# Optimization experiments

Hardware: AMD Instinct MI355X
Metric: run time of the kernel (lower is better)

Reference implementation:

```python
import jax, jax.numpy as jnp
import numpy as np

# Config constants (match init_kwargs)
H = 1024   # hidden_size
F = 4096   # intermediate_size
E = 8      # num_moe_experts
K = 2      # moe_router_topk
S, B = 1024, 2  # seq_len, micro-batch


def setup_inputs() -> dict:
    key = jax.random.key(0)
    ks = jax.random.split(key, 6)
    return {
        "hidden_states": jax.random.normal(ks[0], (S, B, H), jnp.float32),
        "router_w": jax.random.normal(ks[1], (H, E), jnp.float32) * 0.02,
        "w1": jax.random.normal(ks[2], (E, H, F), jnp.float32) * 0.02,
        "b1": jax.random.normal(ks[3], (E, F), jnp.float32) * 0.02,
        "w2": jax.random.normal(ks[4], (E, F, H), jnp.float32) * 0.02,
        "b2": jax.random.normal(ks[5], (E, H), jnp.float32) * 0.02,
    }


def reference(hidden_states, router_w, w1, b1, w2, b2):
    S_, B_, H_ = hidden_states.shape
    x = hidden_states.reshape(-1, H_)                      # [N, H]
    N = x.shape[0]

    # --- TopKRouter (aux_loss routing): topk over logits, softmax over top-k logits ---
    logits = x @ router_w                                  # [N, E]
    top_logits, indices = jax.lax.top_k(logits, K)         # [N, K]
    scores = jax.nn.softmax(top_logits.astype(jnp.float32), axis=-1).astype(logits.dtype)

    # Combine weights [N, E]: scatter top-k scores into expert slots.
    combine = jnp.zeros((N, E), x.dtype).at[jnp.arange(N)[:, None], indices].add(scores)

    # --- Experts: per-expert GPTNeoXMLP (dense over all tokens; math-equivalent
    # to dispatch (token_permutation) + grouped GEMM + scatter_add combine
    # (token_unpermutation) with score weighting for topk>1) ---
    h = jax.nn.gelu(jnp.einsum('nh,ehf->enf', x, w1) + b1[:, None, :], approximate=False)
    y = jnp.einsum('enf,efh->enh', h, w2) + b2[:, None, :]  # [E, N, H]

    out = jnp.einsum('ne,enh->nh', combine, y)              # weighted combine
    return out.reshape(S_, B_, H_)
```

## Files before the change

### kernel.cpp

```cpp
#include <hip/hip_runtime.h>
#include <cmath>


#define H_DIM 1024
#define F_DIM 4096
#define E_NUM 8
#define N_TOK 2048
#define BK 64
#define MAX_SLOTS 5120
#define MAX_MT (MAX_SLOTS / 128)
#define G1_GRID (MAX_MT * 32)
#define G2_GRID (MAX_MT * 16)
#define CVT_BLKS 2048
#define WCHUNKS (E_NUM * H_DIM * F_DIM / 8)
#define XCHUNKS (N_TOK * H_DIM / 8)

typedef short s16x4 __attribute__((ext_vector_type(4)));
typedef short s16x8 __attribute__((ext_vector_type(8)));
typedef float f32x4 __attribute__((ext_vector_type(4)));
typedef __attribute__((address_space(3))) const unsigned short* lds_us;

__device__ __forceinline__ unsigned short f2bf(float f) {
  unsigned int u = __float_as_uint(f);
  u += 0x7fffu + ((u >> 16) & 1u);
  return (unsigned short)(u >> 16);
}

__device__ __forceinline__ void gload_lds16(const void* g, void* l) {
  __builtin_amdgcn_global_load_lds(
      (const __attribute__((address_space(1))) unsigned int*)g,
      (__attribute__((address_space(3))) unsigned int*)l, 16, 0, 0);
}

__device__ __forceinline__ int xcd_swz(int orig, int nwg) {
  const int cpx = nwg >> 3;
  return (orig & 7) * cpx + (orig >> 3);
}

__device__ __forceinline__ float fast_gelu(float v) {
  const float w = v * (1.0f + 0.044715f * v * v);
  const float t = __expf(-1.5957691216f * w);
  return v / (1.0f + t);
}

template<int OFS>
__device__ __forceinline__ s16x4 trread(lds_us p) {
  s16x4 r;
  asm volatile("ds_read_b64_tr_b16 %0, %1 offset:%2" : "=v"(r) : "v"(p), "i"(OFS));
  return r;
}

template<int KB>
__device__ __forceinline__ void ld_b4(lds_us bp, s16x8 bb[4]) {
  s16x4 p0 = trread<KB + 0>(bp),    q0 = trread<KB + 512>(bp);
  s16x4 p1 = trread<KB + 1024>(bp), q1 = trread<KB + 1536>(bp);
  s16x4 p2 = trread<KB + 2048>(bp), q2 = trread<KB + 2560>(bp);
  s16x4 p3 = trread<KB + 3072>(bp), q3 = trread<KB + 3584>(bp);
  bb[0] = __builtin_shufflevector(p0, q0, 0, 1, 2, 3, 4, 5, 6, 7);
  bb[1] = __builtin_shufflevector(p1, q1, 0, 1, 2, 3, 4, 5, 6, 7);
  bb[2] = __builtin_shufflevector(p2, q2, 0, 1, 2, 3, 4, 5, 6, 7);
  bb[3] = __builtin_shufflevector(p3, q3, 0, 1, 2, 3, 4, 5, 6, 7);
}

template<int KB>
__device__ __forceinline__ void ld_b2(lds_us bp, s16x8 bb[2]) {
  s16x4 p0 = trread<KB + 0>(bp),    q0 = trread<KB + 512>(bp);
  s16x4 p1 = trread<KB + 1024>(bp), q1 = trread<KB + 1536>(bp);
  bb[0] = __builtin_shufflevector(p0, q0, 0, 1, 2, 3, 4, 5, 6, 7);
  bb[1] = __builtin_shufflevector(p1, q1, 0, 1, 2, 3, 4, 5, 6, 7);
}

__device__ __forceinline__ void cvt_stream(const float* __restrict__ in,
                                           unsigned short* __restrict__ out,
                                           int blk, int nblk, int nchunks) {
  const int step = nblk * 256;
#pragma unroll 2
  for (int c = blk * 256 + threadIdx.x; c < nchunks; c += step) {
    const size_t i = (size_t)c * 8;
    f32x4 a = *(const f32x4*)(in + i);
    f32x4 b = *(const f32x4*)(in + i + 4);
    s16x8 u;
#pragma unroll
    for (int j = 0; j < 4; ++j) { u[j] = (short)f2bf(a[j]); u[4 + j] = (short)f2bf(b[j]); }
    *(s16x8*)&out[i] = u;
  }
}

__global__ __launch_bounds__(256) void prep_k(
    const float* __restrict__ w1, unsigned short* __restrict__ wbf1,
    const float* __restrict__ x, unsigned short* __restrict__ xb,
    const float* __restrict__ rw, int* __restrict__ topk_e, float* __restrict__ topk_s) {
  const int b = blockIdx.x;
  const int t = threadIdx.x;
  if (b < CVT_BLKS) { cvt_stream(w1, wbf1, b, CVT_BLKS, WCHUNKS); return; }
  if (b < CVT_BLKS + 128) { cvt_stream(x, xb, b - CVT_BLKS, 128, XCHUNKS); return; }
  const int n = (b - CVT_BLKS - 128) * 4 + (t >> 6);
  const int l = t & 63;
  float part[E_NUM];
#pragma unroll
  for (int e = 0; e < E_NUM; ++e) part[e] = 0.f;
  const float* xr = x + (size_t)n * H_DIM;
  for (int h = l; h < H_DIM; h += 64) {
    const float xv = xr[h];
    const float* rwr = rw + h * E_NUM;
#pragma unroll
    for (int e = 0; e < E_NUM; ++e) part[e] += xv * rwr[e];
  }
#pragma unroll
  for (int e = 0; e < E_NUM; ++e) {
#pragma unroll
    for (int off = 32; off > 0; off >>= 1) part[e] += __shfl_down(part[e], off);
  }
  if (l == 0) {
    float v0 = -3.4e38f, v1 = -3.4e38f;
    int i0 = 0, i1 = 0;
#pragma unroll
    for (int e = 0; e < E_NUM; ++e) {
      float v = part[e];
      if (v > v0) { v1 = v0; i1 = i0; v0 = v; i0 = e; }
      else if (v > v1) { v1 = v; i1 = e; }
    }
    const float e1 = expf(v1 - v0);
    const float inv = 1.f / (1.f + e1);
    topk_e[2 * n] = i0; topk_e[2 * n + 1] = i1;
    topk_s[2 * n] = inv; topk_s[2 * n + 1] = e1 * inv;
  }
}

__global__ __launch_bounds__(256) void scatter_k(
    int* __restrict__ meta, const int* __restrict__ topk_e,
    const float* __restrict__ topk_s, int* __restrict__ slot_token,
    float* __restrict__ slot_score) {
  __shared__ int cnt[4][8];
  __shared__ int soff[9];
  __shared__ int scur[8];
  const int t = threadIdx.x;
  const int wv = t >> 6;
  if (t < 32) cnt[t >> 3][t & 7] = 0;
  if (t < 8) scur[t] = 0;
  __syncthreads();
  for (int a = t; a < N_TOK * 2; a += 256)
    atomicAdd(&cnt[wv][topk_e[a]], 1);
  __syncthreads();
  if (t == 0) {
    int acc = 0;
    for (int e = 0; e < E_NUM; ++e) {
      const int c = cnt[0][e] + cnt[1][e] + cnt[2][e] + cnt[3][e];
      soff[e] = acc;
      meta[8 + e] = acc;
      acc += ((c + 127) / 128) * 128;
    }
    soff[8] = acc;
    meta[16] = acc;
  }
  __syncthreads();
  for (int a = t; a < N_TOK * 2; a += 256) {
    const int e = topk_e[a];
    const int pos = atomicAdd(&scur[e], 1);
    const int slot = soff[e] + pos;
    slot_token[slot] = a >> 1;
    slot_score[slot] = topk_s[a];
  }
}

#define KLANE(l) (((l) >> 3 & 3) * 8 + ((l) >> 5) * 4 + (((l) & 7) >> 1))

__global__ __launch_bounds__(256, 2) void gemm1_f(
    const unsigned short* __restrict__ xb, const unsigned short* __restrict__ wbf1,
    const float* __restrict__ b1, const int* __restrict__ meta,
    const int* __restrict__ slot_token, unsigned short* __restrict__ hbuf,
    const float* __restrict__ w2, unsigned short* __restrict__ wbf2) {
  __shared__ __align__(16) unsigned short Al[2 * 8192];
  __shared__ __align__(16) unsigned short Bl[2 * 8192];
  if (blockIdx.x >= G1_GRID) {
    cvt_stream(w2, wbf2, blockIdx.x - G1_GRID, CVT_BLKS, WCHUNKS);
    return;
  }
  const int total = meta[16];
  const int wgid = xcd_swz(blockIdx.x, G1_GRID);
  const int mt = wgid >> 5, nt = wgid & 31;
  const int m0 = mt * 128;
  if (m0 >= total) return;
  int exp = 0;
#pragma unroll
  for (int e = 1; e < E_NUM; ++e) if (m0 >= meta[8 + e]) exp = e;
  const int n0 = nt * 128;
  const int t = threadIdx.x, w = t >> 6, l = t & 63;
  const int wm = w >> 1, wn = w & 1, lr = l & 15, lg = l >> 4;
  const int sr = l >> 3, sc = l & 7;

  const unsigned short* srcA[4];
#pragma unroll
  for (int i = 0; i < 4; ++i) {
    const int r = (w * 4 + i) * 8 + sr;
    int tk = slot_token[m0 + r]; if (tk < 0) tk = 0;
    srcA[i] = xb + (size_t)tk * H_DIM + (sc ^ sr) * 8;
  }
  const unsigned short* wbe = wbf1 + (size_t)exp * H_DIM * F_DIM;
  const unsigned short* srcB[4];
#pragma unroll
  for (int i = 0; i < 4; ++i) {
    const int ri = w * 4 + i;
    const int kl = (ri >> 3) * 32 + KLANE(l);
    srcB[i] = wbe + (size_t)kl * F_DIM + n0 + (ri & 7) * 16 + (l & 1) * 8;
  }

  const f32x4 fzero = {0.f, 0.f, 0.f, 0.f};
  f32x4 acc[4][4];
#pragma unroll
  for (int a = 0; a < 4; ++a)
#pragma unroll
    for (int b = 0; b < 4; ++b) acc[a][b] = fzero;

#define GLA1(kt, Ad)                                                        \
  _Pragma("unroll") for (int i = 0; i < 4; ++i)                             \
      gload_lds16(srcA[i] + (kt) * BK, (Ad) + (w * 4 + i) * 512);
#define GLB1(kt, Bd)                                                        \
  _Pragma("unroll") for (int i = 0; i < 4; ++i)                             \
      gload_lds16(srcB[i] + (size_t)(kt) * (BK * F_DIM), (Bd) + (w * 4 + i) * 512);
#define MFMA1(Ac, Bc)                                                       \
  {                                                                         \
    lds_us bp = (lds_us)(Bc) + wn * 2048 + l * 4;                           \
    _Pragma("unroll") for (int kk = 0; kk < 2; ++kk) {                      \
      s16x8 af[4], bb[4];                                                   \
      _Pragma("unroll") for (int fm = 0; fm < 4; ++fm) {                    \
        const int row = wm * 64 + fm * 16 + lr;                             \
        af[fm] = *(const s16x8*)&(Ac)[row * 64 + (((kk * 4 + lg) ^ (lr & 7)) * 8)]; \
      }                                                                     \
      if (kk == 0) ld_b4<0>(bp, bb); else ld_b4<8192>(bp, bb);              \
      asm volatile("s_waitcnt lgkmcnt(0)" ::: "memory");                    \
      __builtin_amdgcn_sched_barrier(0);                                    \
      _Pragma("unroll") for (int fm = 0; fm < 4; ++fm)                      \
        _Pragma("unroll") for (int fn = 0; fn < 4; ++fn)                    \
          acc[fm][fn] = __builtin_amdgcn_mfma_f32_16x16x32_bf16(af[fm], bb[fn], acc[fm][fn], 0, 0, 0); \
    }                                                                       \
  }

  const int NT = H_DIM / BK;
  GLA1(0, Al) GLB1(0, Bl)
  __syncthreads();
  int cur = 0;
  for (int kt = 0; kt < NT; ++kt) {
    const int nxt = cur ^ 1;
    if (kt + 1 < NT) { GLA1(kt + 1, Al + nxt * 8192) GLB1(kt + 1, Bl + nxt * 8192) }
    MFMA1(Al + cur * 8192, Bl + cur * 8192)
    __syncthreads();
    cur = nxt;
  }
#pragma unroll
  for (int fn = 0; fn < 4; ++fn) {
    const int col = n0 + wn * 64 + fn * 16 + lr;
    const float bias = b1[exp * F_DIM + col];
#pragma unroll
    for (int fm = 0; fm < 4; ++fm) {
      const int rbase = m0 + wm * 64 + fm * 16 + lg * 4;
#pragma unroll
      for (int i = 0; i < 4; ++i) {
        hbuf[(size_t)(rbase + i) * F_DIM + col] = f2bf(fast_gelu(acc[fm][fn][i] + bias));
      }
    }
  }
}

__global__ __launch_bounds__(256, 3) void gemm2_f(
    const unsigned short* __restrict__ hbuf, const unsigned short* __restrict__ wbf2,
    const float* __restrict__ b2, const int* __restrict__ meta,
    const int* __restrict__ slot_token, const float* __restrict__ slot_score,
    float* __restrict__ out) {
  __shared__ __align__(16) unsigned short Al[2 * 8192];
  __shared__ __align__(16) unsigned short Bl[2 * 4096];
  const int total = meta[16];
  const int wgid = xcd_swz(blockIdx.x, G2_GRID);
  const int mt = wgid >> 4, nt = wgid & 15;
  const int m0 = mt * 128;
  if (m0 >= total) return;
  int exp = 0;
#pragma unroll
  for (int e = 1; e < E_NUM; ++e) if (m0 >= meta[8 + e]) exp = e;
  const int n0 = nt * 64;
  const int t = threadIdx.x, w = t >> 6, l = t & 63;
  const int wm = w >> 1, wn = w & 1, lr = l & 15, lg = l >> 4;
  const int sr = l >> 3, sc = l & 7;

  const unsigned short* srcA[4];
#pragma unroll
  for (int i = 0; i < 4; ++i) {
    const int r = (w * 4 + i) * 8 + sr;
    srcA[i] = hbuf + (size_t)(m0 + r) * F_DIM + (sc ^ sr) * 8;
  }
  const unsigned short* wbe = wbf2 + (size_t)exp * F_DIM * H_DIM;
  const unsigned short* srcB[2];
#pragma unroll
  for (int i = 0; i < 2; ++i) {
    const int ri = w * 2 + i;
    const int kl = (ri >> 2) * 32 + KLANE(l);
    srcB[i] = wbe + (size_t)kl * H_DIM + n0 + (ri & 3) * 16 + (l & 1) * 8;
  }

  const f32x4 fzero = {0.f, 0.f, 0.f, 0.f};
  f32x4 acc[4][2];
#pragma unroll
  for (int a = 0; a < 4; ++a)
#pragma unroll
    for (int b = 0; b < 2; ++b) acc[a][b] = fzero;

#define GLA2(kt, Ad)                                                        \
  _Pragma("unroll") for (int i = 0; i < 4; ++i)                             \
      gload_lds16(srcA[i] + (kt) * BK, (Ad) + (w * 4 + i) * 512);
#define GLB2(kt, Bd)                                                        \
  _Pragma("unroll") for (int i = 0; i < 2; ++i)                             \
      gload_lds16(srcB[i] + (size_t)(kt) * (BK * H_DIM), (Bd) + (w * 2 + i) * 512);
#define MFMA2(Ac, Bc)                                                       \
  {                                                                         \
    lds_us bp = (lds_us)(Bc) + wn * 1024 + l * 4;                           \
    _Pragma("unroll") for (int kk = 0; kk < 2; ++kk) {                      \
      s16x8 af[4], bb[2];                                                   \
      _Pragma("unroll") for (int fm = 0; fm < 4; ++fm) {                    \
        const int row = wm * 64 + fm * 16 + lr;                             \
        af[fm] = *(const s16x8*)&(Ac)[row * 64 + (((kk * 4 + lg) ^ (lr & 7)) * 8)]; \
      }                                                                     \
      if (kk == 0) ld_b2<0>(bp, bb); else ld_b2<4096>(bp, bb);              \
      asm volatile("s_waitcnt lgkmcnt(0)" ::: "memory");                    \
      __builtin_amdgcn_sched_barrier(0);                                    \
      _Pragma("unroll") for (int fm = 0; fm < 4; ++fm)                      \
        _Pragma("unroll") for (int fn = 0; fn < 2; ++fn)                    \
          acc[fm][fn] = __builtin_amdgcn_mfma_f32_16x16x32_bf16(af[fm], bb[fn], acc[fm][fn], 0, 0, 0); \
    }                                                                       \
  }

  const int NT = F_DIM / BK;
  GLA2(0, Al) GLB2(0, Bl)
  __syncthreads();
  int cur = 0;
  for (int kt = 0; kt < NT; ++kt) {
    const int nxt = cur ^ 1;
    if (kt + 1 < NT) { GLA2(kt + 1, Al + nxt * 8192) GLB2(kt + 1, Bl + nxt * 4096) }
    MFMA2(Al + cur * 8192, Bl + cur * 4096)
    __syncthreads();
    cur = nxt;
  }
#pragma unroll
  for (int fm = 0; fm < 4; ++fm) {
    const int rbase = m0 + wm * 64 + fm * 16 + lg * 4;
    int toks[4]; float ss[4];
#pragma unroll
    for (int i = 0; i < 4; ++i) {
      toks[i] = slot_token[rbase + i];
      ss[i] = slot_score[rbase + i];
    }
#pragma unroll
    for (int fn = 0; fn < 2; ++fn) {
      const int col = n0 + wn * 32 + fn * 16 + lr;
      const float b2v = b2[exp * H_DIM + col];
#pragma unroll
      for (int i = 0; i < 4; ++i) {
        if (toks[i] >= 0)
          atomicAdd(out + (size_t)toks[i] * H_DIM + col, ss[i] * (acc[fm][fn][i] + b2v));
      }
    }
  }
}

__global__ __launch_bounds__(256) void cvt2_k(const float* __restrict__ in,
                                              unsigned short* __restrict__ out) {
  cvt_stream(in, out, blockIdx.x, CVT_BLKS, WCHUNKS);
}

extern "C" void kernel_launch(void* const* d_in, const int* in_sizes, int n_in,
                              void* d_out, int out_size, void* d_ws, size_t ws_size,
                              hipStream_t stream) {
  const float* x  = (const float*)d_in[0];
  const float* rw = (const float*)d_in[1];
  const float* w1 = (const float*)d_in[2];
  const float* b1 = (const float*)d_in[3];
  const float* w2 = (const float*)d_in[4];
  const float* b2 = (const float*)d_in[5];
  float* out = (float*)d_out;
  char* ws = (char*)d_ws;

  int*   meta       = (int*)ws;
  int*   topk_e     = (int*)(ws + 4096);
  float* topk_s     = (float*)(ws + 20480);
  int*   slot_token = (int*)(ws + 36864);
  float* slot_score = (float*)(ws + 57344);
  unsigned short* xb   = (unsigned short*)(ws + (1ull << 20));
  unsigned short* hbuf = (unsigned short*)(ws + (8ull << 20));
  unsigned short* wbf1 = (unsigned short*)(ws + (48ull << 20));
  const size_t W = (size_t)E_NUM * H_DIM * F_DIM * 2;
  unsigned short* wbf2 = (unsigned short*)(ws + (48ull << 20) + W);
  const bool full = ws_size >= (48ull << 20) + 2 * W;
  if (!full) wbf2 = wbf1;

  hipMemsetAsync(meta, 0, 256, stream);
  hipMemsetAsync(slot_token, 0xFF, MAX_SLOTS * sizeof(int), stream);
  hipMemsetAsync(out, 0, (size_t)N_TOK * H_DIM * sizeof(float), stream);

  prep_k<<<CVT_BLKS + 128 + 512, 256, 0, stream>>>(w1, wbf1, x, xb, rw, topk_e, topk_s);
  scatter_k<<<1, 256, 0, stream>>>(meta, topk_e, topk_s, slot_token, slot_score);

  if (full) {
    gemm1_f<<<G1_GRID + CVT_BLKS, 256, 0, stream>>>(xb, wbf1, b1, meta, slot_token, hbuf, w2, wbf2);
  } else {
    gemm1_f<<<G1_GRID, 256, 0, stream>>>(xb, wbf1, b1, meta, slot_token, hbuf, w2, wbf2);
    cvt2_k<<<CVT_BLKS, 256, 0, stream>>>(w2, wbf2);
  }
  gemm2_f<<<G2_GRID, 256, 0, stream>>>(hbuf, wbf2, b2, meta, slot_token, slot_score, out);
}
```

Baseline: 274.5 us.

## Switch expert GEMMs to BK=32 triple-buffered pipeline with vmcnt-based waits

Both expert GEMM kernels drop from a 64-wide K tile with double buffering and full __syncthreads to a 32-wide K tile with a three-stage LDS ring. Loads run two stages ahead and are tracked with explicit s_waitcnt vmcnt counts plus a bare s_barrier. The smaller LDS footprint lets occupancy hints rise (gemm1 to 3, gemm2 to 4 blocks per CU), and the conversion loop unroll goes from 2 to 4. The aim is to hide global-load latency better and raise occupancy, at the cost of more loop iterations and barriers per K and a fragile manual waitcnt scheme.

```diff
diff --git a/kernel.cpp b/kernel.cpp
--- a/kernel.cpp
+++ b/kernel.cpp
@@ -6,7 +6,7 @@
 #define F_DIM 4096
 #define E_NUM 8
 #define N_TOK 2048
-#define BK 64
+#define BK 32
 #define MAX_SLOTS 5120
 #define MAX_MT (MAX_SLOTS / 128)
 #define G1_GRID (MAX_MT * 32)
@@ -50,22 +50,20 @@
   return r;
 }
 
-template<int KB>
 __device__ __forceinline__ void ld_b4(lds_us bp, s16x8 bb[4]) {
-  s16x4 p0 = trread<KB + 0>(bp),    q0 = trread<KB + 512>(bp);
-  s16x4 p1 = trread<KB + 1024>(bp), q1 = trread<KB + 1536>(bp);
-  s16x4 p2 = trread<KB + 2048>(bp), q2 = trread<KB + 2560>(bp);
-  s16x4 p3 = trread<KB + 3072>(bp), q3 = trread<KB + 3584>(bp);
+  s16x4 p0 = trread<0>(bp),    q0 = trread<512>(bp);
+  s16x4 p1 = trread<1024>(bp), q1 = trread<1536>(bp);
+  s16x4 p2 = trread<2048>(bp), q2 = trread<2560>(bp);
+  s16x4 p3 = trread<3072>(bp), q3 = trread<3584>(bp);
   bb[0] = __builtin_shufflevector(p0, q0, 0, 1, 2, 3, 4, 5, 6, 7);
   bb[1] = __builtin_shufflevector(p1, q1, 0, 1, 2, 3, 4, 5, 6, 7);
   bb[2] = __builtin_shufflevector(p2, q2, 0, 1, 2, 3, 4, 5, 6, 7);
   bb[3] = __builtin_shufflevector(p3, q3, 0, 1, 2, 3, 4, 5, 6, 7);
 }
 
-template<int KB>
 __device__ __forceinline__ void ld_b2(lds_us bp, s16x8 bb[2]) {
-  s16x4 p0 = trread<KB + 0>(bp),    q0 = trread<KB + 512>(bp);
-  s16x4 p1 = trread<KB + 1024>(bp), q1 = trread<KB + 1536>(bp);
+  s16x4 p0 = trread<0>(bp),    q0 = trread<512>(bp);
+  s16x4 p1 = trread<1024>(bp), q1 = trread<1536>(bp);
   bb[0] = __builtin_shufflevector(p0, q0, 0, 1, 2, 3, 4, 5, 6, 7);
   bb[1] = __builtin_shufflevector(p1, q1, 0, 1, 2, 3, 4, 5, 6, 7);
 }
@@ -74,7 +72,7 @@
                                            unsigned short* __restrict__ out,
                                            int blk, int nblk, int nchunks) {
   const int step = nblk * 256;
-#pragma unroll 2
+#pragma unroll 4
   for (int c = blk * 256 + threadIdx.x; c < nchunks; c += step) {
     const size_t i = (size_t)c * 8;
     f32x4 a = *(const f32x4*)(in + i);
@@ -165,13 +163,13 @@
 
 #define KLANE(l) (((l) >> 3 & 3) * 8 + ((l) >> 5) * 4 + (((l) & 7) >> 1))
 
-__global__ __launch_bounds__(256, 2) void gemm1_f(
+__global__ __launch_bounds__(256, 3) void gemm1_f(
     const unsigned short* __restrict__ xb, const unsigned short* __restrict__ wbf1,
     const float* __restrict__ b1, const int* __restrict__ meta,
     const int* __restrict__ slot_token, unsigned short* __restrict__ hbuf,
     const float* __restrict__ w2, unsigned short* __restrict__ wbf2) {
-  __shared__ __align__(16) unsigned short Al[2 * 8192];
-  __shared__ __align__(16) unsigned short Bl[2 * 8192];
+  __shared__ __align__(16) unsigned short Al[3 * 4096];
+  __shared__ __align__(16) unsigned short Bl[3 * 4096];
   if (blockIdx.x >= G1_GRID) {
     cvt_stream(w2, wbf2, blockIdx.x - G1_GRID, CVT_BLKS, WCHUNKS);
     return;
@@ -187,22 +185,17 @@
   const int n0 = nt * 128;
   const int t = threadIdx.x, w = t >> 6, l = t & 63;
   const int wm = w >> 1, wn = w & 1, lr = l & 15, lg = l >> 4;
-  const int sr = l >> 3, sc = l & 7;
-
-  const unsigned short* srcA[4];
-#pragma unroll
-  for (int i = 0; i < 4; ++i) {
-    const int r = (w * 4 + i) * 8 + sr;
-    int tk = slot_token[m0 + r]; if (tk < 0) tk = 0;
-    srcA[i] = xb + (size_t)tk * H_DIM + (sc ^ sr) * 8;
-  }
-  const unsigned short* wbe = wbf1 + (size_t)exp * H_DIM * F_DIM;
-  const unsigned short* srcB[4];
-#pragma unroll
-  for (int i = 0; i < 4; ++i) {
-    const int ri = w * 4 + i;
-    const int kl = (ri >> 3) * 32 + KLANE(l);
-    srcB[i] = wbe + (size_t)kl * F_DIM + n0 + (ri & 7) * 16 + (l & 1) * 8;
+
+  const unsigned short* pA[2];
+  const unsigned short* pB[2];
+#pragma unroll
+  for (int i = 0; i < 2; ++i) {
+    const int q = w * 2 + i;
+    const int row = q * 16 + (l >> 2);
+    int tk = slot_token[m0 + row]; if (tk < 0) tk = 0;
+    pA[i] = xb + (size_t)tk * H_DIM + (((l & 3) ^ ((l >> 3) & 3)) << 3);
+    pB[i] = wbf1 + (size_t)exp * H_DIM * F_DIM + (size_t)KLANE(l) * F_DIM
+            + n0 + q * 16 + (l & 1) * 8;
   }
 
   const f32x4 fzero = {0.f, 0.f, 0.f, 0.f};
@@ -212,41 +205,44 @@
 #pragma unroll
     for (int b = 0; b < 4; ++b) acc[a][b] = fzero;
 
-#define GLA1(kt, Ad)                                                        \
-  _Pragma("unroll") for (int i = 0; i < 4; ++i)                             \
-      gload_lds16(srcA[i] + (kt) * BK, (Ad) + (w * 4 + i) * 512);
-#define GLB1(kt, Bd)                                                        \
-  _Pragma("unroll") for (int i = 0; i < 4; ++i)                             \
-      gload_lds16(srcB[i] + (size_t)(kt) * (BK * F_DIM), (Bd) + (w * 4 + i) * 512);
+  const int fofs = ((lg ^ ((lr >> 1) & 3)) << 3);
+
+#define ISSUE1(Ad, Bd)                                                      \
+  _Pragma("unroll") for (int i = 0; i < 2; ++i) {                           \
+    gload_lds16(pA[i], (Ad) + (w * 2 + i) * 512); pA[i] += BK;              \
+    gload_lds16(pB[i], (Bd) + (w * 2 + i) * 512); pB[i] += (size_t)BK * F_DIM; \
+  }
 #define MFMA1(Ac, Bc)                                                       \
   {                                                                         \
     lds_us bp = (lds_us)(Bc) + wn * 2048 + l * 4;                           \
-    _Pragma("unroll") for (int kk = 0; kk < 2; ++kk) {                      \
-      s16x8 af[4], bb[4];                                                   \
-      _Pragma("unroll") for (int fm = 0; fm < 4; ++fm) {                    \
-        const int row = wm * 64 + fm * 16 + lr;                             \
-        af[fm] = *(const s16x8*)&(Ac)[row * 64 + (((kk * 4 + lg) ^ (lr & 7)) * 8)]; \
-      }                                                                     \
-      if (kk == 0) ld_b4<0>(bp, bb); else ld_b4<8192>(bp, bb);              \
-      asm volatile("s_waitcnt lgkmcnt(0)" ::: "memory");                    \
-      __builtin_amdgcn_sched_barrier(0);                                    \
-      _Pragma("unroll") for (int fm = 0; fm < 4; ++fm)                      \
-        _Pragma("unroll") for (int fn = 0; fn < 4; ++fn)                    \
-          acc[fm][fn] = __builtin_amdgcn_mfma_f32_16x16x32_bf16(af[fm], bb[fn], acc[fm][fn], 0, 0, 0); \
-    }                                                                       \
+    s16x8 af[4], bb[4];                                                     \
+    _Pragma("unroll") for (int fm = 0; fm < 4; ++fm)                        \
+      af[fm] = *(const s16x8*)&(Ac)[(wm * 64 + fm * 16 + lr) * 32 + fofs];  \
+    ld_b4(bp, bb);                                                          \
+    asm volatile("s_waitcnt lgkmcnt(0)" ::: "memory");                      \
+    __builtin_amdgcn_sched_barrier(0);                                      \
+    _Pragma("unroll") for (int fm = 0; fm < 4; ++fm)                        \
+      _Pragma("unroll") for (int fn = 0; fn < 4; ++fn)                      \
+        acc[fm][fn] = __builtin_amdgcn_mfma_f32_16x16x32_bf16(af[fm], bb[fn], acc[fm][fn], 0, 0, 0); \
   }
 
   const int NT = H_DIM / BK;
-  GLA1(0, Al) GLB1(0, Bl)
-  __syncthreads();
+  ISSUE1(Al, Bl)
+  ISSUE1(Al + 4096, Bl + 4096)
   int cur = 0;
   for (int kt = 0; kt < NT; ++kt) {
-    const int nxt = cur ^ 1;
-    if (kt + 1 < NT) { GLA1(kt + 1, Al + nxt * 8192) GLB1(kt + 1, Bl + nxt * 8192) }
-    MFMA1(Al + cur * 8192, Bl + cur * 8192)
-    __syncthreads();
-    cur = nxt;
-  }
+    if (kt + 1 < NT) asm volatile("s_waitcnt vmcnt(4)" ::: "memory");
+    else             asm volatile("s_waitcnt vmcnt(0)" ::: "memory");
+    __builtin_amdgcn_s_barrier();
+    __builtin_amdgcn_sched_barrier(0);
+    if (kt + 2 < NT) {
+      int ib = cur + 2; if (ib >= 3) ib -= 3;
+      ISSUE1(Al + ib * 4096, Bl + ib * 4096)
+    }
+    MFMA1(Al + cur * 4096, Bl + cur * 4096)
+    ++cur; if (cur == 3) cur = 0;
+  }
+
 #pragma unroll
   for (int fn = 0; fn < 4; ++fn) {
     const int col = n0 + wn * 64 + fn * 16 + lr;
@@ -262,13 +258,13 @@
   }
 }
 
-__global__ __launch_bounds__(256, 3) void gemm2_f(
+__global__ __launch_bounds__(256, 4) void gemm2_f(
     const unsigned short* __restrict__ hbuf, const unsigned short* __restrict__ wbf2,
     const float* __restrict__ b2, const int* __restrict__ meta,
     const int* __restrict__ slot_token, const float* __restrict__ slot_score,
     float* __restrict__ out) {
-  __shared__ __align__(16) unsigned short Al[2 * 8192];
-  __shared__ __align__(16) unsigned short Bl[2 * 4096];
+  __shared__ __align__(16) unsigned short Al[3 * 4096];
+  __shared__ __align__(16) unsigned short Bl[3 * 2048];
   const int total = meta[16];
   const int wgid = xcd_swz(blockIdx.x, G2_GRID);
   const int mt = wgid >> 4, nt = wgid & 15;
@@ -280,22 +276,16 @@
   const int n0 = nt * 64;
   const int t = threadIdx.x, w = t >> 6, l = t & 63;
   const int wm = w >> 1, wn = w & 1, lr = l & 15, lg = l >> 4;
-  const int sr = l >> 3, sc = l & 7;
-
-  const unsigned short* srcA[4];
-#pragma unroll
-  for (int i = 0; i < 4; ++i) {
-    const int r = (w * 4 + i) * 8 + sr;
-    srcA[i] = hbuf + (size_t)(m0 + r) * F_DIM + (sc ^ sr) * 8;
-  }
-  const unsigned short* wbe = wbf2 + (size_t)exp * F_DIM * H_DIM;
-  const unsigned short* srcB[2];
+
+  const unsigned short* pA[2];
 #pragma unroll
   for (int i = 0; i < 2; ++i) {
-    const int ri = w * 2 + i;
-    const int kl = (ri >> 2) * 32 + KLANE(l);
-    srcB[i] = wbe + (size_t)kl * H_DIM + n0 + (ri & 3) * 16 + (l & 1) * 8;
-  }
+    const int q = w * 2 + i;
+    const int row = q * 16 + (l >> 2);
+    pA[i] = hbuf + (size_t)(m0 + row) * F_DIM + (((l & 3) ^ ((l >> 3) & 3)) << 3);
+  }
+  const unsigned short* pB = wbf2 + (size_t)exp * F_DIM * H_DIM
+                             + (size_t)KLANE(l) * H_DIM + n0 + w * 16 + (l & 1) * 8;
 
   const f32x4 fzero = {0.f, 0.f, 0.f, 0.f};
   f32x4 acc[4][2];
@@ -304,41 +294,46 @@
 #pragma unroll
     for (int b = 0; b < 2; ++b) acc[a][b] = fzero;
 
-#define GLA2(kt, Ad)                                                        \
-  _Pragma("unroll") for (int i = 0; i < 4; ++i)                             \
-      gload_lds16(srcA[i] + (kt) * BK, (Ad) + (w * 4 + i) * 512);
-#define GLB2(kt, Bd)                                                        \
-  _Pragma("unroll") for (int i = 0; i < 2; ++i)                             \
-      gload_lds16(srcB[i] + (size_t)(kt) * (BK * H_DIM), (Bd) + (w * 2 + i) * 512);
+  const int fofs = ((lg ^ ((lr >> 1) & 3)) << 3);
+
+#define ISSUE2(Ad, Bd)                                                      \
+  {                                                                         \
+    _Pragma("unroll") for (int i = 0; i < 2; ++i) {                         \
+      gload_lds16(pA[i], (Ad) + (w * 2 + i) * 512); pA[i] += BK;            \
+    }                                                                       \
+    gload_lds16(pB, (Bd) + w * 512); pB += (size_t)BK * H_DIM;              \
+  }
 #define MFMA2(Ac, Bc)                                                       \
   {                                                                         \
     lds_us bp = (lds_us)(Bc) + wn * 1024 + l * 4;                           \
-    _Pragma("unroll") for (int kk = 0; kk < 2; ++kk) {                      \
-      s16x8 af[4], bb[2];                                                   \
-      _Pragma("unroll") for (int fm = 0; fm < 4; ++fm) {                    \
-        const int row = wm * 64 + fm * 16 + lr;                             \
-        af[fm] = *(const s16x8*)&(Ac)[row * 64 + (((kk * 4 + lg) ^ (lr & 7)) * 8)]; \
-      }                                                                     \
-      if (kk == 0) ld_b2<0>(bp, bb); else ld_b2<4096>(bp, bb);              \
-      asm volatile("s_waitcnt lgkmcnt(0)" ::: "memory");                    \
-      __builtin_amdgcn_sched_barrier(0);                                    \
-      _Pragma("unroll") for (int fm = 0; fm < 4; ++fm)                      \
-        _Pragma("unroll") for (int fn = 0; fn < 2; ++fn)                    \
-          acc[fm][fn] = __builtin_amdgcn_mfma_f32_16x16x32_bf16(af[fm], bb[fn], acc[fm][fn], 0, 0, 0); \
-    }                                                                       \
+    s16x8 af[4], bb[2];                                                     \
+    _Pragma("unroll") for (int fm = 0; fm < 4; ++fm)                        \
+      af[fm] = *(const s16x8*)&(Ac)[(wm * 64 + fm * 16 + lr) * 32 + fofs];  \
+    ld_b2(bp, bb);                                                          \
+    asm volatile("s_waitcnt lgkmcnt(0)" ::: "memory");                      \
+    __builtin_amdgcn_sched_barrier(0);                                      \
+    _Pragma("unroll") for (int fm = 0; fm < 4; ++fm)                        \
+      _Pragma("unroll") for (int fn = 0; fn < 2; ++fn)                      \
+        acc[fm][fn] = __builtin_amdgcn_mfma_f32_16x16x32_bf16(af[fm], bb[fn], acc[fm][fn], 0, 0, 0); \
   }
 
   const int NT = F_DIM / BK;
-  GLA2(0, Al) GLB2(0, Bl)
-  __syncthreads();
+  ISSUE2(Al, Bl)
+  ISSUE2(Al + 4096, Bl + 2048)
   int cur = 0;
   for (int kt = 0; kt < NT; ++kt) {
-    const int nxt = cur ^ 1;
-    if (kt + 1 < NT) { GLA2(kt + 1, Al + nxt * 8192) GLB2(kt + 1, Bl + nxt * 4096) }
-    MFMA2(Al + cur * 8192, Bl + cur * 4096)
-    __syncthreads();
-    cur = nxt;
-  }
+    if (kt + 1 < NT) asm volatile("s_waitcnt vmcnt(3)" ::: "memory");
+    else             asm volatile("s_waitcnt vmcnt(0)" ::: "memory");
+    __builtin_amdgcn_s_barrier();
+    __builtin_amdgcn_sched_barrier(0);
+    if (kt + 2 < NT) {
+      int ib = cur + 2; if (ib >= 3) ib -= 3;
+      ISSUE2(Al + ib * 4096, Bl + ib * 2048)
+    }
+    MFMA2(Al + cur * 4096, Bl + cur * 2048)
+    ++cur; if (cur == 3) cur = 0;
+  }
+
 #pragma unroll
   for (int fm = 0; fm < 4; ++fm) {
     const int rbase = m0 + wm * 64 + fm * 16 + lg * 4;
```

After: 287.1 us. 1.05x slower.
